# Kernel tuning notes

Hardware: AMD Instinct MI355X
Metric: run time of the kernel (lower is better)

The kernel has to match this reference:

```python
import jax, jax.numpy as jnp
import numpy as np

B, T, D, N = 8, 2048, 1024, 256


def setup_inputs() -> dict:
    key = jax.random.key(0)
    ks = jax.random.split(key, 6)
    sD = 1.0 / np.sqrt(D)
    sN = 1.0 / np.sqrt(N)
    return {
        "x": jax.random.normal(ks[0], (B, T, D), dtype=jnp.float32),
        "Wa": jax.random.normal(ks[1], (D, N), dtype=jnp.float32) * sD,
        "ba": jnp.zeros((N,), jnp.float32),
        "Wb": jax.random.normal(ks[2], (D, N), dtype=jnp.float32) * sD,
        "bb": jnp.zeros((N,), jnp.float32),
        "Wc": jax.random.normal(ks[3], (D, N), dtype=jnp.float32) * sD,
        "bc": jnp.zeros((N,), jnp.float32),
        "Wd": jax.random.normal(ks[4], (D, D), dtype=jnp.float32) * sD,
        "bd": jnp.zeros((D,), jnp.float32),
        "Wy": jax.random.normal(ks[5], (N, D), dtype=jnp.float32) * sN,
        "by": jnp.zeros((D,), jnp.float32),
    }


def reference(x, Wa, ba, Wb, bb, Wc, bc, Wd, bd, Wy, by):
    # Precompute all input-dependent gates/projections in batched GEMMs.
    a = jax.nn.sigmoid(jnp.einsum("btd,dn->btn", x, Wa) + ba)  # (B,T,N)
    b = jnp.einsum("btd,dn->btn", x, Wb) + bb                   # (B,T,N)
    c = jnp.tanh(jnp.einsum("btd,dn->btn", x, Wc) + bc)          # (B,T,N)
    d = jnp.einsum("btd,de->bte", x, Wd) + bd                    # (B,T,D)

    # Sequential linear-gated recurrence: s_t = a_t*s_{t-1} + (1-a_t)*b_t
    def step(s, abc):
        at, bt, ct = abc
        s = at * s + (1.0 - at) * bt
        return s, ct * s

    aT = jnp.swapaxes(a, 0, 1)  # (T,B,N)
    bT = jnp.swapaxes(b, 0, 1)
    cT = jnp.swapaxes(c, 0, 1)
    s0 = jnp.zeros((x.shape[0], Wa.shape[1]), x.dtype)
    _, csT = jax.lax.scan(step, s0, (aT, bT, cT))  # (T,B,N)
    cs = jnp.swapaxes(csT, 0, 1)                    # (B,T,N)

    # Output projection applied once over the full sequence.
    y = jnp.einsum("btn,nd->btd", cs, Wy) + by + d  # (B,T,D)
    return y
```

## Files before the change

kernel.cpp:

```cpp
#include <hip/hip_runtime.h>
#include <hip/hip_bf16.h>

typedef unsigned short u16;
typedef __attribute__((ext_vector_type(8))) short bf16x8;
typedef __attribute__((ext_vector_type(4))) float f32x4;

#define AS1 __attribute__((address_space(1)))
#define AS3 __attribute__((address_space(3)))

#define Bx 8
#define Tt 2048
#define Dd 1024
#define Nn 256
#define Mm (Bx*Tt)
#define CHAINS (Bx*Nn)
#define NCH 32
#define TC 64
#define NCOMB 1792

#define WS_NEED 105644032u

__device__ __forceinline__ u16 f2bf(float f) {
  union { float f; unsigned u; } v; v.f = f;
  unsigned u = v.u;
  u += 0x7fffu + ((u >> 16) & 1u);
  return (u16)(u >> 16);
}

__device__ __forceinline__ float bf2f(u16 h) {
  union { unsigned u; float f; } v; v.u = ((unsigned)h) << 16;
  return v.f;
}

__device__ __forceinline__ void gload_lds16(const void* g, void* l) {
  __builtin_amdgcn_global_load_lds((AS1 void*)(g), (AS3 void*)(l), 16, 0, 0);
}

__global__ void cvt_x_kernel(const float* __restrict__ x, u16* __restrict__ xb) {
  int i = blockIdx.x * blockDim.x + threadIdx.x;
  float4 v = ((const float4*)x)[i];
  unsigned lo = (unsigned)f2bf(v.x) | ((unsigned)f2bf(v.y) << 16);
  unsigned hi = (unsigned)f2bf(v.z) | ((unsigned)f2bf(v.w) << 16);
  ((uint2*)xb)[i] = make_uint2(lo, hi);
}

__global__ void pack_w_kernel(const float* __restrict__ Wa, const float* __restrict__ Wb,
                              const float* __restrict__ Wc, const float* __restrict__ Wd,
                              const float* __restrict__ Wy,
                              u16* __restrict__ Wcomb, u16* __restrict__ Wyt) {
  __shared__ float tile[32][33];
  int z = blockIdx.z;
  const float* src; u16* dst; int R, C, dld;
  if (z < 3)       { src = (z==0?Wa:(z==1?Wb:Wc)); dst = Wcomb + (size_t)z*256*1024; R=1024; C=256;  dld=1024; }
  else if (z == 3) { src = Wd; dst = Wcomb + (size_t)768*1024; R=1024; C=1024; dld=1024; }
  else             { src = Wy; dst = Wyt; R=256;  C=1024; dld=256;  }
  int c0 = blockIdx.x * 32, r0 = blockIdx.y * 32;
  if (c0 >= C || r0 >= R) return;
  int tx = threadIdx.x & 31, ty = threadIdx.x >> 5;
  #pragma unroll
  for (int i = 0; i < 32; i += 8)
    tile[ty + i][tx] = src[(size_t)(r0 + ty + i)*C + (c0 + tx)];
  __syncthreads();
  #pragma unroll
  for (int i = 0; i < 32; i += 8) {
    int c = c0 + ty + i, r = r0 + tx;
    dst[(size_t)c*dld + r] = f2bf(tile[tx][ty + i]);
  }
}

template<int EPI>
__global__ __launch_bounds__(256, 4) void gemm_bt_kernel(
    const u16* __restrict__ A, const u16* __restrict__ Bt, int K,
    u16* __restrict__ outA, float* __restrict__ outO, u16* __restrict__ dtmp,
    const float* __restrict__ b0, const float* __restrict__ b1,
    const float* __restrict__ b2, const float* __restrict__ b3) {
  __shared__ u16 ldsA[128*64];
  __shared__ u16 ldsB[128*64];
  const int tid = threadIdx.x;
  const int lane = tid & 63, wid = tid >> 6;
  const int wr = wid >> 1, wc = wid & 1;
  const int m0 = blockIdx.y * 128, n0 = blockIdx.x * 128;

  f32x4 acc[4][4] = {};

  const int srow = lane >> 3;
  const int sq   = (lane & 7) ^ srow;
  const char* Ab = (const char*)A;
  const char* Bb = (const char*)Bt;

  const int kq  = lane >> 4;
  const int swz = lane & 7;
  const int arow = wr*64 + (lane & 15);
  const int brow = wc*64 + (lane & 15);

  for (int k0 = 0; k0 < K; k0 += 64) {
    #pragma unroll
    for (int i = 0; i < 4; ++i) {
      int g = wid*4 + i;
      int r = g*8 + srow;
      gload_lds16(Ab + ((size_t)(m0 + r)*K + k0 + sq*8)*2, (char*)ldsA + g*1024);
      gload_lds16(Bb + ((size_t)(n0 + r)*K + k0 + sq*8)*2, (char*)ldsB + g*1024);
    }
    __syncthreads();
    #pragma unroll
    for (int kk = 0; kk < 2; ++kk) {
      const int q = ((kk*4 + kq) ^ swz) * 8;
      bf16x8 af[4], bfr[4];
      #pragma unroll
      for (int mi = 0; mi < 4; ++mi)
        af[mi]  = *(const bf16x8*)&ldsA[(arow + mi*16)*64 + q];
      #pragma unroll
      for (int ni = 0; ni < 4; ++ni)
        bfr[ni] = *(const bf16x8*)&ldsB[(brow + ni*16)*64 + q];
      #pragma unroll
      for (int mi = 0; mi < 4; ++mi)
        #pragma unroll
        for (int ni = 0; ni < 4; ++ni)
          acc[mi][ni] = __builtin_amdgcn_mfma_f32_16x16x32_bf16(af[mi], bfr[ni], acc[mi][ni], 0, 0, 0);
    }
    __syncthreads();
  }

  const int crow = m0 + wr*64 + (lane >> 4)*4;
  const int ccol = wc*64 + (lane & 15);
  #pragma unroll
  for (int mi = 0; mi < 4; ++mi) {
    #pragma unroll
    for (int ni = 0; ni < 4; ++ni) {
      int coln = n0 + ccol + ni*16;
      #pragma unroll
      for (int r = 0; r < 4; ++r) {
        int row = crow + mi*16 + r;
        float v = acc[mi][ni][r];
        if (EPI == 0) {
          if (n0 < 768) {
            int seg = coln >> 8, cn = coln & 255;
            if (seg == 0)      v = 1.f / (1.f + __expf(-(v + b0[cn])));
            else if (seg == 1) v = v + b1[cn];
            else               v = tanhf(v + b2[cn]);
            outA[(size_t)row*768 + coln] = f2bf(v);
          } else {
            int col = coln - 768;
            if (dtmp) dtmp[(size_t)row*1024 + col] = f2bf(v + b3[col]);
            else      outO[(size_t)row*1024 + col] = v + b3[col];
          }
        } else {
          const size_t o = (size_t)row*1024 + coln;
          if (dtmp) outO[o] = v + b0[coln] + bf2f(dtmp[o]);
          else      outO[o] = outO[o] + v + b0[coln];
        }
      }
    }
  }
}

__global__ void scanA_kernel(const u16* __restrict__ abc,
                             float* __restrict__ Asum, float* __restrict__ Usum) {
  int idx = blockIdx.x * blockDim.x + threadIdx.x;
  int chain = idx & (CHAINS - 1);
  int ch = idx >> 11;
  int bb = chain >> 8, n = chain & 255;
  const u16* base = abc + (size_t)(bb*Tt + ch*TC) * 768;
  float A = 1.f, U = 0.f;
  for (int t = 0; t < TC; ++t) {
    float a = bf2f(base[(size_t)t*768 + n]);
    float b = bf2f(base[(size_t)t*768 + 256 + n]);
    U = a*U + (1.f - a)*b;
    A *= a;
  }
  Asum[idx] = A; Usum[idx] = U;
}

__global__ void scanB_kernel(const float* __restrict__ Asum, const float* __restrict__ Usum,
                             float* __restrict__ Spre) {
  int chain = blockIdx.x * blockDim.x + threadIdx.x;
  float s = 0.f;
  for (int ch = 0; ch < NCH; ++ch) {
    int i = (ch << 11) + chain;
    Spre[i] = s;
    s = Asum[i]*s + Usum[i];
  }
}

__global__ void scanC_kernel(const u16* __restrict__ abc, const float* __restrict__ Spre,
                             u16* __restrict__ cs) {
  int idx = blockIdx.x * blockDim.x + threadIdx.x;
  int chain = idx & (CHAINS - 1);
  int ch = idx >> 11;
  int bb = chain >> 8, n = chain & 255;
  const u16* base = abc + (size_t)(bb*Tt + ch*TC) * 768;
  u16* csb = cs + (size_t)(bb*Tt + ch*TC) * 256 + n;
  float s = Spre[idx];
  for (int t = 0; t < TC; ++t) {
    float a = bf2f(base[(size_t)t*768 + n]);
    float b = bf2f(base[(size_t)t*768 + 256 + n]);
    float c = bf2f(base[(size_t)t*768 + 512 + n]);
    s = a*s + (1.f - a)*b;
    csb[(size_t)t*256] = f2bf(c*s);
  }
}

extern "C" void kernel_launch(void* const* d_in, const int* in_sizes, int n_in,
                              void* d_out, int out_size, void* d_ws, size_t ws_size,
                              hipStream_t stream) {
  const float* x  = (const float*)d_in[0];
  const float* Wa = (const float*)d_in[1];
  const float* ba = (const float*)d_in[2];
  const float* Wb = (const float*)d_in[3];
  const float* bb = (const float*)d_in[4];
  const float* Wc = (const float*)d_in[5];
  const float* bc = (const float*)d_in[6];
  const float* Wd = (const float*)d_in[7];
  const float* bd = (const float*)d_in[8];
  const float* Wy = (const float*)d_in[9];
  const float* by = (const float*)d_in[10];
  float* out = (float*)d_out;
  char* ws = (char*)d_ws;

  u16*  xb    = (u16*) (ws + 0);
  u16*  Wcomb = (u16*) (ws + 33554432);
  u16*  Wyt   = (u16*) (ws + 37224448);
  u16*  abcb  = (u16*) (ws + 37748736);
  u16*  cs    = (u16*) (ws + 62914560);
  float* Asum = (float*)(ws + 71303168);
  float* Usum = (float*)(ws + 71565312);
  float* Spre = (float*)(ws + 71827456);
  u16*  dtmp  = (ws_size >= WS_NEED) ? (u16*)(ws + 72089600) : nullptr;

  cvt_x_kernel<<<Mm*Dd/4/256, 256, 0, stream>>>(x, xb);
  pack_w_kernel<<<dim3(32, 32, 5), 256, 0, stream>>>(Wa, Wb, Wc, Wd, Wy, Wcomb, Wyt);
  gemm_bt_kernel<0><<<dim3(NCOMB/128, Mm/128), 256, 0, stream>>>(
      xb, Wcomb, Dd, abcb, out, dtmp, ba, bb, bc, bd);
  scanA_kernel<<<CHAINS*NCH/256, 256, 0, stream>>>(abcb, Asum, Usum);
  scanB_kernel<<<CHAINS/256, 256, 0, stream>>>(Asum, Usum, Spre);
  scanC_kernel<<<CHAINS*NCH/256, 256, 0, stream>>>(abcb, Spre, cs);
  gemm_bt_kernel<2><<<dim3(Dd/128, Mm/128), 256, 0, stream>>>(
      cs, Wyt, Nn, nullptr, out, dtmp, by, nullptr, nullptr, nullptr);
}
```

Measured before the change: 170.4 us.

## Enlarge GEMM tiles to 256x128 with 512 threads and XCD-aware block remap

```diff
diff --git a/kernel.cpp b/kernel.cpp
--- a/kernel.cpp
+++ b/kernel.cpp
@@ -69,42 +69,48 @@
 }
 
 template<int EPI>
-__global__ __launch_bounds__(256, 4) void gemm_bt_kernel(
-    const u16* __restrict__ A, const u16* __restrict__ Bt, int K,
+__global__ __launch_bounds__(512, 4) void gemm_bt_kernel(
+    const u16* __restrict__ A, const u16* __restrict__ Bt, int K, int gx,
     u16* __restrict__ outA, float* __restrict__ outO, u16* __restrict__ dtmp,
     const float* __restrict__ b0, const float* __restrict__ b1,
     const float* __restrict__ b2, const float* __restrict__ b3) {
-  __shared__ u16 ldsA[128*64];
+  __shared__ u16 ldsA[256*64];
   __shared__ u16 ldsB[128*64];
   const int tid = threadIdx.x;
   const int lane = tid & 63, wid = tid >> 6;
-  const int wr = wid >> 1, wc = wid & 1;
-  const int m0 = blockIdx.y * 128, n0 = blockIdx.x * 128;
+  const int wm = wid >> 1, wn = wid & 1;
+
+  const int h = blockIdx.x;
+  const int id = (h & 7) * (gridDim.x >> 3) + (h >> 3);
+  const int mt = id / gx, nt = id % gx;
+  const int m0 = mt * 256, n0 = nt * 128;
 
   f32x4 acc[4][4] = {};
 
-  const int srow = lane >> 3;
-  const int sq   = (lane & 7) ^ srow;
-  const char* Ab = (const char*)A;
-  const char* Bb = (const char*)Bt;
-
-  const int kq  = lane >> 4;
-  const int swz = lane & 7;
-  const int arow = wr*64 + (lane & 15);
-  const int brow = wc*64 + (lane & 15);
+  const int rl  = tid >> 3;
+  const int ssl = (tid & 7) ^ (rl & 7);
+
+  auto stage = [&](int k0) {
+    #pragma unroll
+    for (int u = 0; u < 4; ++u)
+      gload_lds16(A + (size_t)(m0 + u*64 + rl)*K + k0 + ssl*8,
+                  ldsA + u*4096 + tid*8);
+    #pragma unroll
+    for (int u = 0; u < 2; ++u)
+      gload_lds16(Bt + (size_t)(n0 + u*64 + rl)*K + k0 + ssl*8,
+                  ldsB + u*4096 + tid*8);
+  };
+
+  const int lr = lane & 15, kq = lane >> 4, sw = lane & 7;
+  const int arow = wm*64 + lr;
+  const int brow = wn*64 + lr;
 
   for (int k0 = 0; k0 < K; k0 += 64) {
-    #pragma unroll
-    for (int i = 0; i < 4; ++i) {
-      int g = wid*4 + i;
-      int r = g*8 + srow;
-      gload_lds16(Ab + ((size_t)(m0 + r)*K + k0 + sq*8)*2, (char*)ldsA + g*1024);
-      gload_lds16(Bb + ((size_t)(n0 + r)*K + k0 + sq*8)*2, (char*)ldsB + g*1024);
-    }
+    stage(k0);
     __syncthreads();
     #pragma unroll
     for (int kk = 0; kk < 2; ++kk) {
-      const int q = ((kk*4 + kq) ^ swz) * 8;
+      const int q = ((kk*4 + kq) ^ sw) * 8;
       bf16x8 af[4], bfr[4];
       #pragma unroll
       for (int mi = 0; mi < 4; ++mi)
@@ -121,8 +127,8 @@
     __syncthreads();
   }
 
-  const int crow = m0 + wr*64 + (lane >> 4)*4;
-  const int ccol = wc*64 + (lane & 15);
+  const int crow = m0 + wm*64 + (lane >> 4)*4;
+  const int ccol = wn*64 + (lane & 15);
   #pragma unroll
   for (int mi = 0; mi < 4; ++mi) {
     #pragma unroll
@@ -133,7 +139,7 @@
         int row = crow + mi*16 + r;
         float v = acc[mi][ni][r];
         if (EPI == 0) {
-          if (n0 < 768) {
+          if (coln < 768) {
             int seg = coln >> 8, cn = coln & 255;
             if (seg == 0)      v = 1.f / (1.f + __expf(-(v + b0[cn])));
             else if (seg == 1) v = v + b1[cn];
@@ -229,11 +235,11 @@
 
   cvt_x_kernel<<<Mm*Dd/4/256, 256, 0, stream>>>(x, xb);
   pack_w_kernel<<<dim3(32, 32, 5), 256, 0, stream>>>(Wa, Wb, Wc, Wd, Wy, Wcomb, Wyt);
-  gemm_bt_kernel<0><<<dim3(NCOMB/128, Mm/128), 256, 0, stream>>>(
-      xb, Wcomb, Dd, abcb, out, dtmp, ba, bb, bc, bd);
+  gemm_bt_kernel<0><<<896, 512, 0, stream>>>(
+      xb, Wcomb, Dd, NCOMB/128, abcb, out, dtmp, ba, bb, bc, bd);
   scanA_kernel<<<CHAINS*NCH/256, 256, 0, stream>>>(abcb, Asum, Usum);
   scanB_kernel<<<CHAINS/256, 256, 0, stream>>>(Asum, Usum, Spre);
   scanC_kernel<<<CHAINS*NCH/256, 256, 0, stream>>>(abcb, Spre, cs);
-  gemm_bt_kernel<2><<<dim3(Dd/128, Mm/128), 256, 0, stream>>>(
-      cs, Wyt, Nn, nullptr, out, dtmp, by, nullptr, nullptr, nullptr);
-}
+  gemm_bt_kernel<2><<<512, 512, 0, stream>>>(
+      cs, Wyt, Nn, Dd/128, nullptr, out, dtmp, by, nullptr, nullptr, nullptr);
+}
```

Measured after the change: 156.1 us. 8.4% less time.
